# Optimization experiments

Hardware: AMD Instinct MI355X
Metric: run time of the kernel (lower is better)

Reference implementation:

```python
import jax, jax.numpy as jnp
import numpy as np

D = 1024
H = 16
HD = D // H  # 64

def setup_inputs() -> dict:
    key = jax.random.key(0)
    ks = jax.random.split(key, 7)
    B, S = 2, 2048
    x = jax.random.normal(ks[0], (B, S, D), dtype=jnp.float32)
    M = jax.random.randint(ks[1], (B, S, S), 0, 2, dtype=jnp.int32)
    s = 1.0 / np.sqrt(D)
    W_q = jax.random.normal(ks[2], (D, D), dtype=jnp.float32) * s
    W_k = jax.random.normal(ks[3], (D, D), dtype=jnp.float32) * s
    W_v = jax.random.normal(ks[4], (D, D), dtype=jnp.float32) * s
    W_o = jax.random.normal(ks[5], (D, D), dtype=jnp.float32) * s
    b_o = jax.random.normal(ks[6], (D,), dtype=jnp.float32) * 0.01
    return {"x": x, "M": M, "W_q": W_q, "W_k": W_k, "W_v": W_v, "W_o": W_o, "b_o": b_o}

def reference(x, M, W_q, W_k, W_v, W_o, b_o):
    B, S, _ = x.shape
    scale = HD ** -0.5
    # project and split heads: [B, H, S, HD]
    def heads(W):
        return (x @ W.T).reshape(B, S, H, HD).transpose(0, 2, 1, 3)
    Q, K, V = heads(W_q), heads(W_k), heads(W_v)
    scores = jnp.einsum('bhqd,bhkd->bhqk', Q, K) * scale
    mask = (M[:, None, :, :] == 0)  # broadcast over heads
    scores = jnp.where(mask, jnp.float32(-1e9), scores)
    A = jax.nn.softmax(scores, axis=-1)
    out = jnp.einsum('bhqk,bhkd->bhqd', A, V)
    out = out.transpose(0, 2, 1, 3).reshape(B, S, D)
    return out @ W_o.T + b_o
```

## Files before the change

kernel.cpp:

```cpp
#include <hip/hip_runtime.h>
#include <hip/hip_bf16.h>

typedef unsigned short u16;
typedef unsigned int u32;
typedef unsigned long long u64;
typedef _Float16 f16;
typedef __attribute__((__ext_vector_type__(4))) _Float16 f16x4;
typedef __attribute__((__ext_vector_type__(8))) short bf16x8;
typedef __attribute__((__ext_vector_type__(4))) float f32x4;
typedef __attribute__((__ext_vector_type__(16))) float f32x16;
typedef __attribute__((__ext_vector_type__(2))) int i32x2;

__device__ __forceinline__ u16 f2bf(float f) {
    u32 u = __float_as_uint(f);
    return (u16)((u + 0x7fffu + ((u >> 16) & 1u)) >> 16);
}

__global__ __launch_bounds__(256) void prep_kernel(
    const float4* __restrict__ x,  const float4* __restrict__ wq,
    const float4* __restrict__ wk, const float4* __restrict__ wv,
    const float4* __restrict__ wo,
    u16* __restrict__ xb, u16* __restrict__ wqb, u16* __restrict__ wkb,
    u16* __restrict__ wvb, u16* __restrict__ wob,
    const int* __restrict__ M, u64* __restrict__ Mb2)
{
    if (blockIdx.x < 8192) {
        int gid = blockIdx.x * 256 + threadIdx.x;
        const float4* src; u16* dst; int off;
        if (gid < 1048576) { src = x; dst = xb; off = gid; }
        else {
            int g = gid - 1048576;
            int sel = g >> 18;
            off = g & 262143;
            src = sel == 0 ? wq : sel == 1 ? wk : sel == 2 ? wv : wo;
            dst = sel == 0 ? wqb : sel == 1 ? wkb : sel == 2 ? wvb : wob;
        }
        float4 f = src[off];
        ushort4 o;
        o.x = f2bf(f.x); o.y = f2bf(f.y); o.z = f2bf(f.z); o.w = f2bf(f.w);
        ((ushort4*)dst)[off] = o;
    } else {
        int wg   = (blockIdx.x - 8192) * 4 + (threadIdx.x >> 6);
        int lane = threadIdx.x & 63;
        int w = wg & 31;
        int q = (wg >> 5) & 2047;
        int b = wg >> 16;
        size_t base = ((size_t)(b * 2048 + q)) * 2048 + w * 64 + lane;
        u64 bits = __ballot(M[base] != 0);
        if (lane == 0) Mb2[(size_t)(b * 32 + w) * 2048 + q] = bits;
    }
}

template<int MODE, int BN>
__global__ __launch_bounds__(256) void gemm_k(
    const u16* __restrict__ Ag, const u16* __restrict__ Bg,
    u16* __restrict__ Cq, u16* __restrict__ Kfr, u16* __restrict__ Vfr,
    float* __restrict__ Cf, const float* __restrict__ bias)
{
    constexpr int Kd = 1024;
    constexpr int NB = BN / 32;
    __shared__ u16 SM[8192 + BN * 64];
    u16* As0 = SM;
    u16* As1 = SM + 4096;
    u16* Bs0 = SM + 8192;
    u16* Bs1 = SM + 8192 + BN * 32;
    const int tid  = threadIdx.x;
    const int wave = tid >> 6, lane = tid & 63;
    const int quad = lane >> 4, l16 = lane & 15;
    const int n0 = blockIdx.x * BN;
    const int m0 = blockIdx.y * 128;

    const int wm = (wave & 1) * 64, wn = (wave >> 1) * (BN / 2);
    f32x4 acc[4][NB];
    #pragma unroll
    for (int i = 0; i < 4; i++)
        #pragma unroll
        for (int j = 0; j < NB; j++)
            acc[i][j] = (f32x4){0.f, 0.f, 0.f, 0.f};

    const int sr = lane >> 2;
    const int sk = (lane & 3) * 8;
    const int ca0 = wave * 2, ca1 = ca0 + 1;
    const u16* gA0 = Ag + (size_t)(m0 + ca0 * 16 + sr) * Kd + sk;
    const u16* gA1 = Ag + (size_t)(m0 + ca1 * 16 + sr) * Kd + sk;
    const int cb0 = (BN == 128) ? wave * 2 : wave;
    const u16* gB0 = Bg + (size_t)(n0 + cb0 * 16 + sr) * Kd + sk;
    const u16* gB1 = (BN == 128) ? Bg + (size_t)(n0 + (cb0 + 1) * 16 + sr) * Kd + sk : nullptr;

    #define GLL16(gp, lp) __builtin_amdgcn_global_load_lds( \
        (const __attribute__((address_space(1))) void*)(gp), \
        (__attribute__((address_space(3))) void*)(lp), 16, 0, 0)

    for (int k0 = 0; k0 < Kd; k0 += 64) {
        __syncthreads();
        GLL16(gA0 + k0, As0 + ca0 * 512);
        GLL16(gA1 + k0, As0 + ca1 * 512);
        GLL16(gB0 + k0, Bs0 + cb0 * 512);
        if (BN == 128) GLL16(gB1 + k0, Bs0 + (cb0 + 1) * 512);
        GLL16(gA0 + k0 + 32, As1 + ca0 * 512);
        GLL16(gA1 + k0 + 32, As1 + ca1 * 512);
        GLL16(gB0 + k0 + 32, Bs1 + cb0 * 512);
        if (BN == 128) GLL16(gB1 + k0 + 32, Bs1 + (cb0 + 1) * 512);
        __syncthreads();

        #pragma unroll
        for (int kk = 0; kk < 2; kk++) {
            const u16* Ah = kk ? As1 : As0;
            const u16* Bh = kk ? Bs1 : Bs0;
            bf16x8 af[4], bfr[NB];
            #pragma unroll
            for (int mb = 0; mb < 4; mb++)
                af[mb] = *(const bf16x8*)&Ah[(wm + mb * 16 + l16) * 32 + quad * 8];
            #pragma unroll
            for (int nb = 0; nb < NB; nb++)
                bfr[nb] = *(const bf16x8*)&Bh[(wn + nb * 16 + l16) * 32 + quad * 8];
            #pragma unroll
            for (int mb = 0; mb < 4; mb++)
                #pragma unroll
                for (int nb = 0; nb < NB; nb++)
                    acc[mb][nb] = __builtin_amdgcn_mfma_f32_16x16x32_bf16(
                        af[mb], bfr[nb], acc[mb][nb], 0, 0, 0);
        }
    }
    #undef GLL16

    if (MODE == 1) {
        #pragma unroll
        for (int mb = 0; mb < 4; mb++)
            #pragma unroll
            for (int nb = 0; nb < NB; nb++) {
                const int row = m0 + wm + mb * 16 + quad * 4;
                const int col = n0 + wn + nb * 16 + l16;
                #pragma unroll
                for (int r = 0; r < 4; r++)
                    Cf[(size_t)(row + r) * 1024 + col] = acc[mb][nb][r] + bias[col];
            }
        return;
    }

    const int region = n0 >> 10;
    if (region == 0) {
        #pragma unroll
        for (int mb = 0; mb < 4; mb++)
            #pragma unroll
            for (int nb = 0; nb < NB; nb++) {
                const int row = m0 + wm + mb * 16 + quad * 4;
                const int ccol = (n0 & 1023) + wn + nb * 16 + l16;
                #pragma unroll
                for (int r = 0; r < 4; r++)
                    Cq[(size_t)(row + r) * 1024 + ccol] =
                        f2bf(acc[mb][nb][r] * 0.18033688011112042f);
            }
        return;
    }

    const int bb = m0 >> 11;
    const int kt_base = (m0 & 2047) >> 6;
    const int head_base = (n0 & 1023) >> 6;
    u16* dst = (region == 1) ? Kfr : Vfr;
    #pragma unroll
    for (int pass = 0; pass < 2; pass++) {
        __syncthreads();
        #pragma unroll
        for (int mb = 0; mb < 4; mb++) {
            const int rowb = wm + mb * 16 + quad * 4;
            if ((rowb >> 6) != pass) continue;
            #pragma unroll
            for (int nb = 0; nb < NB; nb++) {
                const int ccol = wn + nb * 16 + l16;
                const int h2 = ccol >> 6, dd = ccol & 63;
                if (region == 1) {
                    const int t = dd >> 4, hik = (dd >> 3) & 1, j = dd & 7;
                    #pragma unroll
                    for (int r = 0; r < 4; r++) {
                        const int km = (rowb + r) & 63;
                        const int f = (km >> 5) * 4 + t;
                        const int lanek = hik * 32 + (km & 31);
                        SM[((h2 * 8 + f) * 64 + lanek) * 8 + j] = f2bf(acc[mb][nb][r]);
                    }
                } else {
                    const int kinb = rowb & 63;
                    const int t = kinb >> 4, hiv = (kinb >> 3) & 1, jb = kinb & 7;
                    const int f = (dd >> 5) * 4 + t;
                    const int lanev = hiv * 32 + (dd & 31);
                    ushort4 pk;
                    pk.x = f2bf(acc[mb][nb][0]); pk.y = f2bf(acc[mb][nb][1]);
                    pk.z = f2bf(acc[mb][nb][2]); pk.w = f2bf(acc[mb][nb][3]);
                    *(ushort4*)&SM[((h2 * 8 + f) * 64 + lanev) * 8 + jb] = pk;
                }
            }
        }
        __syncthreads();
        const int h2g = tid >> 7;
        const int inner = (tid & 127) * 32;
        const size_t gbase =
            ((size_t)(bb * 16 + head_base + h2g) * 32 + kt_base + pass) * 4096;
        #pragma unroll
        for (int c = 0; c < 4; c++)
            *(bf16x8*)&dst[gbase + inner + c * 8] =
                *(const bf16x8*)&SM[h2g * 4096 + inner + c * 8];
    }
}

__global__ __launch_bounds__(256, 2) void attn_kernel(
    const u16* __restrict__ Qg, const u16* __restrict__ Kfr, const u16* __restrict__ Vfr,
    const u64* __restrict__ Mb2, u16* __restrict__ AO)
{
    const int qt = blockIdx.x;
    const int h  = blockIdx.y;
    const int b  = blockIdx.z;
    const int tid = threadIdx.x, wave = tid >> 6, lane = tid & 63;
    const int l31 = lane & 31, hi = lane >> 5;
    const int pair = wave >> 1;
    const int kh   = wave & 1;

    const int qrow0 = qt * 128 + pair * 64;
    const int bh    = b * 16 + h;

    bf16x8 qfa[4], qfb[4];
    {
        const u16* qp = Qg + ((size_t)b * 2048 + qrow0 + l31) * 1024 + h * 64 + hi * 8;
        #pragma unroll
        for (int t = 0; t < 4; t++) qfa[t] = *(const bf16x8*)(qp + t * 16);
        #pragma unroll
        for (int t = 0; t < 4; t++) qfb[t] = *(const bf16x8*)(qp + 32 * 1024 + t * 16);
    }

    const u32 fro = (u32)bh * 131072u + (u32)lane * 8u;
    const u64* mp = Mb2 + (size_t)(b * 32) * 2048 + qrow0 + l31;

    bf16x8 ones;
    #pragma unroll
    for (int j = 0; j < 8; j++) ones[j] = (short)0x3F80;

    f32x16 oa0, oa1, ob0, ob1, la, lb;
    #pragma unroll
    for (int i = 0; i < 16; i++) {
        oa0[i] = 0.f; oa1[i] = 0.f; ob0[i] = 0.f; ob1[i] = 0.f;
        la[i] = 0.f;  lb[i] = 0.f;
    }

    const int kt0 = kh * 16;
    #pragma unroll 1
    for (int kt = kt0; kt < kt0 + 16; ++kt) {
        const u64 mwa = mp[(size_t)kt * 2048];
        const u64 mwb = mp[(size_t)kt * 2048 + 32];
        const u32 fb = fro + (u32)kt * 4096u;

        #pragma unroll
        for (int ph = 0; ph < 2; ph++) {
            bf16x8 kf[4], vf[4];
            #pragma unroll
            for (int t = 0; t < 4; t++)
                kf[t] = *(const bf16x8*)(Kfr + fb + (u32)(ph * 4 + t) * 512u);
            vf[0] = *(const bf16x8*)(Vfr + fb + (u32)(2 * ph) * 512u);
            vf[1] = *(const bf16x8*)(Vfr + fb + (u32)(2 * ph + 1) * 512u);
            vf[2] = *(const bf16x8*)(Vfr + fb + (u32)(4 + 2 * ph) * 512u);
            vf[3] = *(const bf16x8*)(Vfr + fb + (u32)(4 + 2 * ph + 1) * 512u);

            const u32 mna = ~((ph ? (u32)(mwa >> 32) : (u32)mwa) >> (hi * 4));
            const u32 mnb = ~((ph ? (u32)(mwb >> 32) : (u32)mwb) >> (hi * 4));
            f32x16 sa, sb;
            #pragma unroll
            for (int reg = 0; reg < 16; reg++) {
                const int kb2 = (reg & 3) + 8 * (reg >> 2);
                sa[reg] = __int_as_float(
                    __builtin_amdgcn_sbfe((int)mna, kb2, 1) & (int)0xFF800000);
                sb[reg] = __int_as_float(
                    __builtin_amdgcn_sbfe((int)mnb, kb2, 1) & (int)0xFF800000);
            }
            #pragma unroll
            for (int t = 0; t < 4; t++) {
                sa = __builtin_amdgcn_mfma_f32_32x32x16_bf16(kf[t], qfa[t], sa, 0, 0, 0);
                sb = __builtin_amdgcn_mfma_f32_32x32x16_bf16(kf[t], qfb[t], sb, 0, 0, 0);
            }

            u32 wa[8], wb[8];
            #pragma unroll
            for (int i = 0; i < 8; i++) {
                const float ea0 = __builtin_amdgcn_exp2f(sa[2 * i]);
                const float ea1 = __builtin_amdgcn_exp2f(sa[2 * i + 1]);
                wa[i] = __builtin_amdgcn_perm(__float_as_uint(ea1),
                                              __float_as_uint(ea0), 0x07060302u);
                const float eb0 = __builtin_amdgcn_exp2f(sb[2 * i]);
                const float eb1 = __builtin_amdgcn_exp2f(sb[2 * i + 1]);
                wb[i] = __builtin_amdgcn_perm(__float_as_uint(eb1),
                                              __float_as_uint(eb0), 0x07060302u);
            }

            bf16x8 pba[2], pbb[2];
            #pragma unroll
            for (int fl = 0; fl < 2; fl++) {
                i32x2 a02 = __builtin_amdgcn_permlane32_swap(
                    (int)wa[4 * fl + 0], (int)wa[4 * fl + 2], false, false);
                i32x2 a13 = __builtin_amdgcn_permlane32_swap(
                    (int)wa[4 * fl + 1], (int)wa[4 * fl + 3], false, false);
                union { u32 u[4]; bf16x8 v; } fa;
                fa.u[0] = (u32)a02[0]; fa.u[1] = (u32)a13[0];
                fa.u[2] = (u32)a02[1]; fa.u[3] = (u32)a13[1];
                pba[fl] = fa.v;
                i32x2 b02 = __builtin_amdgcn_permlane32_swap(
                    (int)wb[4 * fl + 0], (int)wb[4 * fl + 2], false, false);
                i32x2 b13 = __builtin_amdgcn_permlane32_swap(
                    (int)wb[4 * fl + 1], (int)wb[4 * fl + 3], false, false);
                union { u32 u[4]; bf16x8 v; } fbu;
                fbu.u[0] = (u32)b02[0]; fbu.u[1] = (u32)b13[0];
                fbu.u[2] = (u32)b02[1]; fbu.u[3] = (u32)b13[1];
                pbb[fl] = fbu.v;
            }

            oa0 = __builtin_amdgcn_mfma_f32_32x32x16_bf16(vf[0], pba[0], oa0, 0, 0, 0);
            ob0 = __builtin_amdgcn_mfma_f32_32x32x16_bf16(vf[0], pbb[0], ob0, 0, 0, 0);
            oa0 = __builtin_amdgcn_mfma_f32_32x32x16_bf16(vf[1], pba[1], oa0, 0, 0, 0);
            ob0 = __builtin_amdgcn_mfma_f32_32x32x16_bf16(vf[1], pbb[1], ob0, 0, 0, 0);
            oa1 = __builtin_amdgcn_mfma_f32_32x32x16_bf16(vf[2], pba[0], oa1, 0, 0, 0);
            ob1 = __builtin_amdgcn_mfma_f32_32x32x16_bf16(vf[2], pbb[0], ob1, 0, 0, 0);
            oa1 = __builtin_amdgcn_mfma_f32_32x32x16_bf16(vf[3], pba[1], oa1, 0, 0, 0);
            ob1 = __builtin_amdgcn_mfma_f32_32x32x16_bf16(vf[3], pbb[1], ob1, 0, 0, 0);
            la  = __builtin_amdgcn_mfma_f32_32x32x16_bf16(ones,  pba[0], la,  0, 0, 0);
            lb  = __builtin_amdgcn_mfma_f32_32x32x16_bf16(ones,  pbb[0], lb,  0, 0, 0);
            la  = __builtin_amdgcn_mfma_f32_32x32x16_bf16(ones,  pba[1], la,  0, 0, 0);
            lb  = __builtin_amdgcn_mfma_f32_32x32x16_bf16(ones,  pbb[1], lb,  0, 0, 0);
        }
    }

    __shared__ float MRG[2 * 64 * 68];
    float* slot = &MRG[(pair * 64 + lane) * 68];
    if (kh == 1) {
        #pragma unroll
        for (int i = 0; i < 4; i++) {
            *(f32x4*)(slot +      4 * i) = (f32x4){oa0[4*i], oa0[4*i+1], oa0[4*i+2], oa0[4*i+3]};
            *(f32x4*)(slot + 16 + 4 * i) = (f32x4){oa1[4*i], oa1[4*i+1], oa1[4*i+2], oa1[4*i+3]};
            *(f32x4*)(slot + 32 + 4 * i) = (f32x4){ob0[4*i], ob0[4*i+1], ob0[4*i+2], ob0[4*i+3]};
            *(f32x4*)(slot + 48 + 4 * i) = (f32x4){ob1[4*i], ob1[4*i+1], ob1[4*i+2], ob1[4*i+3]};
        }
        slot[64] = la[0];
        slot[65] = lb[0];
    }
    __syncthreads();
    if (kh == 0) {
        #pragma unroll
        for (int i = 0; i < 16; i++) {
            oa0[i] += slot[i];
            oa1[i] += slot[16 + i];
            ob0[i] += slot[32 + i];
            ob1[i] += slot[48 + i];
        }
        const float invA = 1.0f / (la[0] + slot[64]);
        const float invB = 1.0f / (lb[0] + slot[65]);
        const size_t qbase = ((size_t)b * 2048 + qrow0 + l31) * 1024 + h * 64;
        #pragma unroll
        for (int tile = 0; tile < 2; tile++) {
            #pragma unroll
            for (int g = 0; g < 4; g++) {
                const int d0 = tile * 32 + g * 8 + hi * 4;
                ushort4 pa, pb;
                #pragma unroll
                for (int r = 0; r < 4; r++) {
                    const int reg = g * 4 + r;
                    const float va = (tile == 0 ? oa0[reg] : oa1[reg]) * invA;
                    const float vb = (tile == 0 ? ob0[reg] : ob1[reg]) * invB;
                    ((u16*)&pa)[r] = f2bf(va);
                    ((u16*)&pb)[r] = f2bf(vb);
                }
                *(ushort4*)&AO[qbase + d0] = pa;
                *(ushort4*)&AO[qbase + (size_t)32 * 1024 + d0] = pb;
            }
        }
    }
}

extern "C" void kernel_launch(void* const* d_in, const int* in_sizes, int n_in,
                              void* d_out, int out_size, void* d_ws, size_t ws_size,
                              hipStream_t stream)
{
    const float* x  = (const float*)d_in[0];
    const int*   Mm = (const int*)d_in[1];
    const float* Wq = (const float*)d_in[2];
    const float* Wk = (const float*)d_in[3];
    const float* Wv = (const float*)d_in[4];
    const float* Wo = (const float*)d_in[5];
    const float* bo = (const float*)d_in[6];
    float* out = (float*)d_out;

    u16* ws  = (u16*)d_ws;
    u16* xb  = ws;
    u16* wqb = xb  + 4194304;
    u16* wkb = wqb + 1048576;
    u16* wvb = wkb + 1048576;
    u16* wob = wvb + 1048576;
    u16* Qb  = wob + 1048576;
    u16* Kfr = Qb  + 4194304;
    u16* Vfr = Kfr + 4194304;
    u16* AOb = Vfr + 4194304;
    u64* Mb2 = (u64*)(AOb + 4194304);

    prep_kernel<<<40960, 256, 0, stream>>>(
        (const float4*)x, (const float4*)Wq, (const float4*)Wk,
        (const float4*)Wv, (const float4*)Wo, xb, wqb, wkb, wvb, wob,
        Mm, Mb2);

    dim3 g1(24, 32, 1);
    gemm_k<0, 128><<<g1, 256, 0, stream>>>(xb, wqb, Qb, Kfr, Vfr, nullptr, nullptr);

    dim3 g2(16, 16, 2);
    attn_kernel<<<g2, 256, 0, stream>>>(Qb, Kfr, Vfr, Mb2, AOb);

    dim3 g3(16, 32, 1);
    gemm_k<1, 64><<<g3, 256, 0, stream>>>(AOb, wob, nullptr, nullptr, nullptr,
                                          out, bo);
}
```

Baseline: 232.6 us.

## Double-buffer GEMM LDS tiles with prefetch and raise priority around attention MFMAs

The projection GEMM now uses two LDS buffers. It issues global-to-LDS loads for the next K tile before computing on the current one, with one barrier per iteration instead of two. This overlaps memory latency with MFMA work but doubles shared memory per block, which can lower occupancy. The attention loop also wraps its MFMA groups in s_setprio to favor waves issuing matrix instructions.

```diff
diff --git a/kernel.cpp b/kernel.cpp
--- a/kernel.cpp
+++ b/kernel.cpp
@@ -59,11 +59,8 @@
 {
     constexpr int Kd = 1024;
     constexpr int NB = BN / 32;
-    __shared__ u16 SM[8192 + BN * 64];
-    u16* As0 = SM;
-    u16* As1 = SM + 4096;
-    u16* Bs0 = SM + 8192;
-    u16* Bs1 = SM + 8192 + BN * 32;
+    constexpr int BUF = 8192 + BN * 64;
+    __shared__ u16 SM[2 * BUF];
     const int tid  = threadIdx.x;
     const int wave = tid >> 6, lane = tid & 63;
     const int quad = lane >> 4, l16 = lane & 15;
@@ -91,22 +88,34 @@
         (const __attribute__((address_space(1))) void*)(gp), \
         (__attribute__((address_space(3))) void*)(lp), 16, 0, 0)
 
+    #define STAGE(K0, BASE)                                            \
+    {                                                                  \
+        u16* As0_ = (BASE);                                            \
+        u16* As1_ = (BASE) + 4096;                                     \
+        u16* Bs0_ = (BASE) + 8192;                                     \
+        u16* Bs1_ = (BASE) + 8192 + BN * 32;                           \
+        GLL16(gA0 + (K0), As0_ + ca0 * 512);                           \
+        GLL16(gA1 + (K0), As0_ + ca1 * 512);                           \
+        GLL16(gB0 + (K0), Bs0_ + cb0 * 512);                           \
+        if (BN == 128) GLL16(gB1 + (K0), Bs0_ + (cb0 + 1) * 512);      \
+        GLL16(gA0 + (K0) + 32, As1_ + ca0 * 512);                      \
+        GLL16(gA1 + (K0) + 32, As1_ + ca1 * 512);                      \
+        GLL16(gB0 + (K0) + 32, Bs1_ + cb0 * 512);                      \
+        if (BN == 128) GLL16(gB1 + (K0) + 32, Bs1_ + (cb0 + 1) * 512); \
+    }
+
+    STAGE(0, SM);
+    __syncthreads();
+
     for (int k0 = 0; k0 < Kd; k0 += 64) {
-        __syncthreads();
-        GLL16(gA0 + k0, As0 + ca0 * 512);
-        GLL16(gA1 + k0, As0 + ca1 * 512);
-        GLL16(gB0 + k0, Bs0 + cb0 * 512);
-        if (BN == 128) GLL16(gB1 + k0, Bs0 + (cb0 + 1) * 512);
-        GLL16(gA0 + k0 + 32, As1 + ca0 * 512);
-        GLL16(gA1 + k0 + 32, As1 + ca1 * 512);
-        GLL16(gB0 + k0 + 32, Bs1 + cb0 * 512);
-        if (BN == 128) GLL16(gB1 + k0 + 32, Bs1 + (cb0 + 1) * 512);
-        __syncthreads();
+        u16* cur = SM + ((k0 >> 6) & 1) * BUF;
+        u16* nxt = SM + (((k0 >> 6) & 1) ^ 1) * BUF;
+        if (k0 + 64 < Kd) STAGE(k0 + 64, nxt);
 
         #pragma unroll
         for (int kk = 0; kk < 2; kk++) {
-            const u16* Ah = kk ? As1 : As0;
-            const u16* Bh = kk ? Bs1 : Bs0;
+            const u16* Ah = cur + (kk ? 4096 : 0);
+            const u16* Bh = cur + 8192 + (kk ? BN * 32 : 0);
             bf16x8 af[4], bfr[NB];
             #pragma unroll
             for (int mb = 0; mb < 4; mb++)
@@ -121,7 +130,9 @@
                     acc[mb][nb] = __builtin_amdgcn_mfma_f32_16x16x32_bf16(
                         af[mb], bfr[nb], acc[mb][nb], 0, 0, 0);
         }
-    }
+        __syncthreads();
+    }
+    #undef STAGE
     #undef GLL16
 
     if (MODE == 1) {
@@ -269,11 +280,13 @@
                 sb[reg] = __int_as_float(
                     __builtin_amdgcn_sbfe((int)mnb, kb2, 1) & (int)0xFF800000);
             }
+            __builtin_amdgcn_s_setprio(1);
             #pragma unroll
             for (int t = 0; t < 4; t++) {
                 sa = __builtin_amdgcn_mfma_f32_32x32x16_bf16(kf[t], qfa[t], sa, 0, 0, 0);
                 sb = __builtin_amdgcn_mfma_f32_32x32x16_bf16(kf[t], qfb[t], sb, 0, 0, 0);
             }
+            __builtin_amdgcn_s_setprio(0);
 
             u32 wa[8], wb[8];
             #pragma unroll
@@ -309,6 +322,7 @@
                 pbb[fl] = fbu.v;
             }
 
+            __builtin_amdgcn_s_setprio(1);
             oa0 = __builtin_amdgcn_mfma_f32_32x32x16_bf16(vf[0], pba[0], oa0, 0, 0, 0);
             ob0 = __builtin_amdgcn_mfma_f32_32x32x16_bf16(vf[0], pbb[0], ob0, 0, 0, 0);
             oa0 = __builtin_amdgcn_mfma_f32_32x32x16_bf16(vf[1], pba[1], oa0, 0, 0, 0);
@@ -321,6 +335,7 @@
             lb  = __builtin_amdgcn_mfma_f32_32x32x16_bf16(ones,  pbb[0], lb,  0, 0, 0);
             la  = __builtin_amdgcn_mfma_f32_32x32x16_bf16(ones,  pba[1], la,  0, 0, 0);
             lb  = __builtin_amdgcn_mfma_f32_32x32x16_bf16(ones,  pbb[1], lb,  0, 0, 0);
+            __builtin_amdgcn_s_setprio(0);
         }
     }
 
```

After: 218.0 us. -6.3%, faster.
